# Kernel optimization log

Measured on AMD Instinct MI355X. Metric: run time of the kernel, lower is better.

## Reference

```python
import jax, jax.numpy as jnp
import numpy as np

H = 128; B = 128; NA = 32; N = B * NA; NH = 4; DH = H // NH; F = 2 * H + 3


def _ln(x, g, b, eps=1e-5):
    m = x.mean(-1, keepdims=True)
    v = ((x - m) ** 2).mean(-1, keepdims=True)
    return (x - m) / jnp.sqrt(v + eps) * g + b


def _silu(x):
    return x * jax.nn.sigmoid(x)


def setup_inputs() -> dict:
    key = jax.random.key(0)
    ks = jax.random.split(key, 16)
    def rn(i, shape, s=0.05):
        return jax.random.normal(ks[i], shape, jnp.float32) * s
    return dict(
        num_atoms=jnp.full((B,), NA, dtype=jnp.int32),
        elems=jax.random.randint(ks[0], (N,), 0, 119),
        cell=jnp.tile(10.0 * jnp.eye(3, dtype=jnp.float32), (B, 1)),  # [3B,3]
        coord=jax.random.uniform(ks[1], (N, 3), jnp.float32, 1.0, 9.0),
        emb=rn(2, (119, H), 1.0),
        ln_in_g=jnp.ones((H,), jnp.float32), ln_in_b=jnp.zeros((H,), jnp.float32),
        attn_in_w=rn(3, (H, 3 * H)), attn_in_b=jnp.zeros((3 * H,), jnp.float32),
        attn_out_w=rn(4, (H, H)), attn_out_b=jnp.zeros((H,), jnp.float32),
        ce_w1=rn(5, (3, H)), ce_b1=jnp.zeros((H,), jnp.float32),
        ce_w2=rn(6, (H, H)), ce_b2=jnp.zeros((H,), jnp.float32),
        ln_feat_g=jnp.ones((F,), jnp.float32), ln_feat_b=jnp.zeros((F,), jnp.float32),
        op_w1=rn(7, (F, H)), op_b1=jnp.zeros((H,), jnp.float32),
        op_ln1_g=jnp.ones((H,), jnp.float32), op_ln1_b=jnp.zeros((H,), jnp.float32),
        res_w1=rn(8, (H, H)), res_b1=jnp.zeros((H,), jnp.float32),
        res_ln_g=jnp.ones((H,), jnp.float32), res_ln_b=jnp.zeros((H,), jnp.float32),
        res_w2=rn(9, (H, H)), res_b2=jnp.zeros((H,), jnp.float32),
        op_ln2_g=jnp.ones((H,), jnp.float32), op_ln2_b=jnp.zeros((H,), jnp.float32),
        op_w3=rn(10, (H, 3)), op_b3=jnp.zeros((3,), jnp.float32),
    )


def reference(num_atoms, elems, cell, coord, emb, ln_in_g, ln_in_b,
              attn_in_w, attn_in_b, attn_out_w, attn_out_b,
              ce_w1, ce_b1, ce_w2, ce_b2, ln_feat_g, ln_feat_b,
              op_w1, op_b1, op_ln1_g, op_ln1_b,
              res_w1, res_b1, res_ln_g, res_ln_b, res_w2, res_b2,
              op_ln2_g, op_ln2_b, op_w3, op_b3):
    n = coord.shape[0]
    # atom embedding + input LayerNorm
    x = _ln(emb[elems], ln_in_g, ln_in_b)
    # unbatched multihead self-attention over all atoms (seq_len = n)
    qkv = x @ attn_in_w + attn_in_b
    q, k, v = jnp.split(qkv, 3, axis=-1)
    q = q.reshape(n, NH, DH); k = k.reshape(n, NH, DH); v = v.reshape(n, NH, DH)
    a = jax.nn.softmax(jnp.einsum('qhd,khd->hqk', q, k) / np.float32(np.sqrt(DH)), axis=-1)
    x = jnp.einsum('hqk,khd->qhd', a, v).reshape(n, H) @ attn_out_w + attn_out_b
    # cell encoder on [3B,3] rows
    cf = _silu(cell @ ce_w1 + ce_b1) @ ce_w2 + ce_b2
    bidx = jnp.repeat(jnp.arange(num_atoms.shape[0]), num_atoms, total_repeat_length=n)
    # torch: cf.repeat(B,1)[batch_idx] == cf[batch_idx] since batch_idx < B
    comb = _ln(jnp.concatenate([x, cf[bidx], coord], axis=-1), ln_feat_g, ln_feat_b)
    # offset predictor
    h = _silu(_ln(comb @ op_w1 + op_b1, op_ln1_g, op_ln1_b))
    h = h + (_silu(_ln(h @ res_w1 + res_b1, res_ln_g, res_ln_b)) @ res_w2 + res_b2)
    h = _ln(h, op_ln2_g, op_ln2_b)
    offset = jnp.tanh(h @ op_w3 + op_b3) * 0.01
    perturbed = coord + offset
    # per-molecule clamp: segment gather of per-cell-row min/max replaces the python loop
    c3 = cell.reshape(-1, 3, 3)           # [B,3,3]
    cmin = c3.min(axis=2) + 1e-6          # [B,3]
    cmax = c3.max(axis=2) - 1e-6          # [B,3]
    return jnp.clip(perturbed, cmin[bidx], cmax[bidx])
```

## Files before the change

kernel.cpp:

```cpp
#include <hip/hip_runtime.h>
#include <hip/hip_bf16.h>
#include <math.h>
#include <stdint.h>

#define NATOMS 4096
#define HD     128
#define NHEAD  4
#define DHEAD  32
#define FDIM   259
#define BATCH  128
#define H3X    384
#define SPLIT  4

typedef __attribute__((ext_vector_type(8))) short short8;
typedef __attribute__((ext_vector_type(4))) float float4v;
typedef __attribute__((ext_vector_type(16))) float f32x16;

__device__ __forceinline__ ushort f2bf(float f) {
    uint32_t u = __float_as_uint(f);
    return (ushort)((u + 0x7fffu + ((u >> 16) & 1u)) >> 16);
}
__device__ __forceinline__ float b2f(ushort u) {
    return __uint_as_float(((uint32_t)u) << 16);
}
__device__ __forceinline__ f32x16 z16() {
    f32x16 v;
#pragma unroll
    for (int i = 0; i < 16; i++) v[i] = 0.f;
    return v;
}

__device__ __forceinline__ float blk_sum_128(float v, float* scratch) {
#pragma unroll
    for (int o = 32; o; o >>= 1) v += __shfl_down(v, o);
    int lane = threadIdx.x & 63, w = threadIdx.x >> 6;
    if (lane == 0) scratch[w] = v;
    __syncthreads();
    float r = scratch[0] + scratch[1];
    __syncthreads();
    return r;
}

#define NB_EMB 1024
#define NB_PACK 528
#define NB_CELL 128
__global__ __launch_bounds__(256) void k_setup(
        const int* __restrict__ num_atoms, const float* __restrict__ cell,
        const int* __restrict__ elems, const float* __restrict__ emb,
        const float* __restrict__ ln_in_g, const float* __restrict__ ln_in_b,
        const float* __restrict__ qkvw, const float* __restrict__ aow,
        const float* __restrict__ op1w, const float* __restrict__ r1w,
        const float* __restrict__ r2w,
        const float* __restrict__ ce_w1, const float* __restrict__ ce_b1,
        const float* __restrict__ ce_w2, const float* __restrict__ ce_b2,
        int* __restrict__ bidx, float* __restrict__ cmin, float* __restrict__ cmax,
        ushort* __restrict__ Xb, ushort* __restrict__ Wqkv, ushort* __restrict__ Wao,
        ushort* __restrict__ Wop1, ushort* __restrict__ Wr1, ushort* __restrict__ Wr2,
        float* __restrict__ CF) {
    __shared__ float hs[HD];
    __shared__ int start[BATCH + 1];
    const int t = threadIdx.x, w = t >> 6, lane = t & 63;
    if (blockIdx.x < NB_EMB) {
        int row = blockIdx.x * 4 + w;
        int e = elems[row];
        float v0 = emb[e * HD + lane], v1 = emb[e * HD + 64 + lane];
        float s = v0 + v1, ss = v0 * v0 + v1 * v1;
#pragma unroll
        for (int m = 1; m < 64; m <<= 1) { s += __shfl_xor(s, m); ss += __shfl_xor(ss, m); }
        float mean = s * (1.f / HD);
        float var = ss * (1.f / HD) - mean * mean;
        float inv = rsqrtf(var + 1e-5f);
        Xb[row * HD + lane] = f2bf((v0 - mean) * inv * ln_in_g[lane] + ln_in_b[lane]);
        Xb[row * HD + 64 + lane] = f2bf((v1 - mean) * inv * ln_in_g[64 + lane] + ln_in_b[64 + lane]);
    } else if (blockIdx.x < NB_EMB + NB_PACK) {
        int idx = (blockIdx.x - NB_EMB) * 256 + t;
        if (idx < 49152) {
            int n = idx >> 7, k = idx & 127;
            Wqkv[idx] = f2bf(qkvw[k * H3X + n]);
        } else if (idx < 65536) {
            int j = idx - 49152; int n = j >> 7, k = j & 127;
            Wao[j] = f2bf(aow[k * HD + n]);
        } else if (idx < 102400) {
            int j = idx - 65536; int n = j / 288, k = j - n * 288;
            Wop1[j] = (k < FDIM) ? f2bf(op1w[k * HD + n]) : (ushort)0;
        } else if (idx < 118784) {
            int j = idx - 102400; int n = j >> 7, k = j & 127;
            Wr1[j] = f2bf(r1w[k * HD + n]);
        } else if (idx < 135168) {
            int j = idx - 118784; int n = j >> 7, k = j & 127;
            Wr2[j] = f2bf(r2w[k * HD + n]);
        }
    } else if (blockIdx.x < NB_EMB + NB_PACK + NB_CELL) {
        int r = blockIdx.x - (NB_EMB + NB_PACK);
        if (t < 128) {
            float c0 = cell[r * 3 + 0], c1 = cell[r * 3 + 1], c2 = cell[r * 3 + 2];
            float h = c0 * ce_w1[t] + c1 * ce_w1[HD + t] + c2 * ce_w1[2 * HD + t] + ce_b1[t];
            h = h / (1.f + __expf(-h));
            hs[t] = h;
        }
        __syncthreads();
        if (t < 128) {
            float acc = ce_b2[t];
#pragma unroll 8
            for (int k = 0; k < HD; k++) acc += hs[k] * ce_w2[k * HD + t];
            CF[r * HD + t] = acc;
        }
    } else {
        if (t == 0) {
            int pos = 0;
            for (int b = 0; b < BATCH; b++) { start[b] = pos; pos += num_atoms[b]; }
            start[BATCH] = pos;
        }
        __syncthreads();
        if (t < 128) {
            int s = min(start[t], NATOMS), e = min(start[t + 1], NATOMS);
            for (int j = s; j < e; j++) bidx[j] = t;
            if (t == 0) {
                int total = min(start[BATCH], NATOMS);
                for (int j = total; j < NATOMS; j++) bidx[j] = BATCH - 1;
            }
        }
        for (int rr = t; rr < BATCH * 3; rr += 256) {
            float a0 = cell[rr * 3 + 0], a1 = cell[rr * 3 + 1], a2 = cell[rr * 3 + 2];
            cmin[rr] = fminf(a0, fminf(a1, a2)) + 1e-6f;
            cmax[rr] = fmaxf(a0, fmaxf(a1, a2)) - 1e-6f;
        }
    }
}

__global__ __launch_bounds__(256) void k_qkv(const ushort* __restrict__ A,
                                             const ushort* __restrict__ Wt,
                                             const float* __restrict__ bias,
                                             ushort* __restrict__ Qb, ushort* __restrict__ Kb,
                                             ushort* __restrict__ VTb) {
    __shared__ alignas(16) ushort vt_tmp[4][128][16];
    const int t = threadIdx.x, w = t >> 6, lane = t & 63, quad = lane >> 4, lq = lane & 15;
    const int rowbase = blockIdx.x * 64 + w * 16;
    float4v acc[24];
#pragma unroll
    for (int i = 0; i < 24; i++) acc[i] = (float4v){0.f, 0.f, 0.f, 0.f};
#pragma unroll
    for (int kt = 0; kt < 4; kt++) {
        short8 af = *(const short8*)(A + (rowbase + lq) * HD + kt * 32 + quad * 8);
#pragma unroll
        for (int nt = 0; nt < 24; nt++) {
            short8 wf = *(const short8*)(Wt + (lq + 16 * nt) * HD + kt * 32 + quad * 8);
            acc[nt] = __builtin_amdgcn_mfma_f32_16x16x32_bf16(af, wf, acc[nt], 0, 0, 0);
        }
    }
#pragma unroll
    for (int nt = 0; nt < 24; nt++) {
        int col = lq + 16 * nt;
        float bb = bias[col];
#pragma unroll
        for (int r = 0; r < 4; r++) {
            float c = acc[nt][r] + bb;
            int row = rowbase + quad * 4 + r;
            if (nt < 8) {
                Qb[(((col >> 5) * NATOMS) + row) * 32 + (col & 31)] = f2bf(c * 0.25503487f);
            } else if (nt < 16) {
                int cc = col - 128;
                Kb[(((cc >> 5) * NATOMS) + row) * 32 + (cc & 31)] = f2bf(c);
            } else {
                int cc = col - 256;
                vt_tmp[w][cc][quad * 4 + r] = f2bf(c);
            }
        }
    }
#pragma unroll
    for (int pass = 0; pass < 2; pass++) {
        int cc = lane + 64 * pass;
        int hh = cc >> 5, d = cc & 31;
        uint4 a0 = *(const uint4*)&vt_tmp[w][cc][0];
        uint4 a1 = *(const uint4*)&vt_tmp[w][cc][8];
        ushort* dst = VTb + (size_t)(hh * 32 + d) * NATOMS + rowbase;
        *(uint4*)(dst) = a0;
        *(uint4*)(dst + 8) = a1;
    }
}

__global__ __launch_bounds__(256) void k_attn(const ushort* __restrict__ Qb,
                                              const ushort* __restrict__ Kb,
                                              const ushort* __restrict__ VTb,
                                              ushort* __restrict__ Opart,
                                              float* __restrict__ lpart) {
    __shared__ alignas(16) ushort P_s[4][32 * 72];
    __shared__ alignas(16) float OL[2][32 * 36];
    __shared__ float LL[2][32];
    const int t = threadIdx.x, w = t >> 6, lane = t & 63;
    const int l31 = lane & 31, hi = lane >> 5;
    const int qt = w & 1, kh2 = w >> 1;
    const int h = blockIdx.y, sp = blockIdx.z;
    const int q0 = blockIdx.x * 64;
    const int qrow = q0 + qt * 32 + l31;

    short8 qf0 = *(const short8*)(Qb + (size_t)(h * NATOMS + qrow) * 32 + hi * 8);
    short8 qf1 = *(const short8*)(Qb + (size_t)(h * NATOMS + qrow) * 32 + 16 + hi * 8);
    f32x16 O = z16();
    float lp = 0.f;
    ushort* Pw = &P_s[w][0];
    const int kstart = sp * (NATOMS / SPLIT) + kh2 * 64;

    for (int ck = 0; ck < (NATOMS / SPLIT) / 128; ck++) {
        int kb = kstart + ck * 128;
#pragma unroll
        for (int kt = 0; kt < 2; kt++) {
            int kk = kb + kt * 32;
            const ushort* kp = Kb + (size_t)(h * NATOMS + kk + l31) * 32 + hi * 8;
            short8 kf0 = *(const short8*)(kp);
            short8 kf1 = *(const short8*)(kp + 16);
            f32x16 S = z16();
            S = __builtin_amdgcn_mfma_f32_32x32x16_bf16(kf0, qf0, S, 0, 0, 0);
            S = __builtin_amdgcn_mfma_f32_32x32x16_bf16(kf1, qf1, S, 0, 0, 0);
#pragma unroll
            for (int c = 0; c < 4; c++) {
                float p0 = exp2f(S[4 * c + 0]);
                float p1 = exp2f(S[4 * c + 1]);
                float p2 = exp2f(S[4 * c + 2]);
                float p3 = exp2f(S[4 * c + 3]);
                lp += (p0 + p1) + (p2 + p3);
                uint2 u;
                u.x = (uint32_t)f2bf(p0) | ((uint32_t)f2bf(p1) << 16);
                u.y = (uint32_t)f2bf(p2) | ((uint32_t)f2bf(p3) << 16);
                *(uint2*)(&Pw[l31 * 72 + kt * 32 + c * 8 + hi * 4]) = u;
            }
#pragma unroll
            for (int wd = 0; wd < 2; wd++) {
                int koff = kt * 32 + wd * 16;
                short8 vf = *(const short8*)(VTb + (size_t)(h * 32 + l31) * NATOMS + kb + koff + hi * 8);
                short8 pf = *(const short8*)(&Pw[l31 * 72 + koff + hi * 8]);
                O = __builtin_amdgcn_mfma_f32_32x32x16_bf16(vf, pf, O, 0, 0, 0);
            }
        }
    }
    lp += __shfl_xor(lp, 32);
    if (kh2 == 0) {
#pragma unroll
        for (int c = 0; c < 4; c++) {
            float4 f = {O[4 * c + 0], O[4 * c + 1], O[4 * c + 2], O[4 * c + 3]};
            *(float4*)(&OL[qt][l31 * 36 + c * 8 + hi * 4]) = f;
        }
        if (hi == 0) LL[qt][l31] = lp;
    }
    __syncthreads();
    if (kh2 == 1) {
        lp += LL[qt][l31];
#pragma unroll
        for (int c = 0; c < 4; c++) {
            float4 f = *(const float4*)(&OL[qt][l31 * 36 + c * 8 + hi * 4]);
            float o0 = O[4 * c + 0] + f.x, o1 = O[4 * c + 1] + f.y;
            float o2 = O[4 * c + 2] + f.z, o3 = O[4 * c + 3] + f.w;
            uint2 u;
            u.x = (uint32_t)f2bf(o0) | ((uint32_t)f2bf(o1) << 16);
            u.y = (uint32_t)f2bf(o2) | ((uint32_t)f2bf(o3) << 16);
            *(uint2*)(Opart + (size_t)(sp * NATOMS + qrow) * HD + h * 32 + c * 8 + hi * 4) = u;
        }
        if (hi == 0) lpart[sp * (NHEAD * NATOMS) + h * NATOMS + qrow] = lp;
    }
}

__global__ __launch_bounds__(256) void k_ao(const ushort* __restrict__ Opart,
                                            const float* __restrict__ lpart,
                                            const ushort* __restrict__ Wt,
                                            const float* __restrict__ bias,
                                            ushort* __restrict__ X1b) {
    const int t = threadIdx.x, w = t >> 6, lane = t & 63, quad = lane >> 4, lq = lane & 15;
    const int rowbase = blockIdx.x * 64 + w * 16;
    const int arow = rowbase + lq;
    float4v acc[8];
#pragma unroll
    for (int i = 0; i < 8; i++) acc[i] = (float4v){0.f, 0.f, 0.f, 0.f};
#pragma unroll
    for (int kt = 0; kt < 4; kt++) {
        float l = 0.f;
#pragma unroll
        for (int s = 0; s < SPLIT; s++) l += lpart[s * (NHEAD * NATOMS) + kt * NATOMS + arow];
        float inv = 1.f / l;
        float pv[8];
#pragma unroll
        for (int j = 0; j < 8; j++) pv[j] = 0.f;
#pragma unroll
        for (int s = 0; s < SPLIT; s++) {
            short8 ov = *(const short8*)(Opart + (size_t)(s * NATOMS + arow) * HD + kt * 32 + quad * 8);
#pragma unroll
            for (int j = 0; j < 8; j++) pv[j] += b2f((ushort)ov[j]);
        }
        short8 af;
#pragma unroll
        for (int j = 0; j < 8; j++) af[j] = (short)f2bf(pv[j] * inv);
#pragma unroll
        for (int nt = 0; nt < 8; nt++) {
            short8 wf = *(const short8*)(Wt + (lq + 16 * nt) * HD + kt * 32 + quad * 8);
            acc[nt] = __builtin_amdgcn_mfma_f32_16x16x32_bf16(af, wf, acc[nt], 0, 0, 0);
        }
    }
#pragma unroll
    for (int r = 0; r < 4; r++) {
        int row = rowbase + quad * 4 + r;
#pragma unroll
        for (int nt = 0; nt < 8; nt++)
            X1b[(size_t)row * HD + lq + 16 * nt] = f2bf(acc[nt][r] + bias[lq + 16 * nt]);
    }
}

__global__ void k_comb(const ushort* __restrict__ X1b, const float* __restrict__ CF,
                       const float* __restrict__ coord, const int* __restrict__ bidx,
                       const float* __restrict__ g, const float* __restrict__ b,
                       ushort* __restrict__ COMBb) {
    __shared__ float sc[2];
    int row = blockIdx.x, t = threadIdx.x;
    int bi = bidx[row];
    float v0 = b2f(X1b[row * HD + t]);
    float v1 = CF[bi * HD + t];
    float v2 = (t < 3) ? coord[row * 3 + t] : 0.f;
    float tot = blk_sum_128(v0 + v1 + v2, sc);
    float mean = tot * (1.f / FDIM);
    float d0 = v0 - mean, d1 = v1 - mean, d2 = (t < 3) ? (v2 - mean) : 0.f;
    float var = blk_sum_128(d0 * d0 + d1 * d1 + d2 * d2, sc) * (1.f / FDIM);
    float inv = rsqrtf(var + 1e-5f);
    COMBb[row * 288 + t] = f2bf(d0 * inv * g[t] + b[t]);
    COMBb[row * 288 + 128 + t] = f2bf(d1 * inv * g[128 + t] + b[128 + t]);
    if (t < 3) COMBb[row * 288 + 256 + t] = f2bf(d2 * inv * g[256 + t] + b[256 + t]);
    if (t >= 3 && t < 32) COMBb[row * 288 + 256 + t] = 0;
}

__global__ __launch_bounds__(256) void k_op1(const ushort* __restrict__ A,
                                             const ushort* __restrict__ Wt,
                                             const float* __restrict__ bias,
                                             const float* __restrict__ lg,
                                             const float* __restrict__ lb,
                                             ushort* __restrict__ out) {
    const int t = threadIdx.x, w = t >> 6, lane = t & 63, quad = lane >> 4, lq = lane & 15;
    const int rowbase = blockIdx.x * 64 + w * 16;
    float4v acc[8];
#pragma unroll
    for (int i = 0; i < 8; i++) acc[i] = (float4v){0.f, 0.f, 0.f, 0.f};
#pragma unroll
    for (int kt = 0; kt < 9; kt++) {
        short8 af = *(const short8*)(A + (size_t)(rowbase + lq) * 288 + kt * 32 + quad * 8);
#pragma unroll
        for (int nt = 0; nt < 8; nt++) {
            short8 wf = *(const short8*)(Wt + (size_t)(lq + 16 * nt) * 288 + kt * 32 + quad * 8);
            acc[nt] = __builtin_amdgcn_mfma_f32_16x16x32_bf16(af, wf, acc[nt], 0, 0, 0);
        }
    }
#pragma unroll
    for (int r = 0; r < 4; r++) {
        float c[8], s1 = 0.f, s2 = 0.f;
#pragma unroll
        for (int nt = 0; nt < 8; nt++) {
            c[nt] = acc[nt][r] + bias[lq + 16 * nt];
            s1 += c[nt]; s2 += c[nt] * c[nt];
        }
#pragma unroll
        for (int m = 1; m < 16; m <<= 1) { s1 += __shfl_xor(s1, m); s2 += __shfl_xor(s2, m); }
        float mean = s1 * (1.f / HD);
        float var = s2 * (1.f / HD) - mean * mean;
        float inv = rsqrtf(var + 1e-5f);
        int row = rowbase + quad * 4 + r;
#pragma unroll
        for (int nt = 0; nt < 8; nt++) {
            float o = (c[nt] - mean) * inv * lg[lq + 16 * nt] + lb[lq + 16 * nt];
            o = o / (1.f + __expf(-o));
            out[(size_t)row * HD + lq + 16 * nt] = f2bf(o);
        }
    }
}

__global__ __launch_bounds__(256) void k_tail(const ushort* __restrict__ Hb,
        const ushort* __restrict__ Wr1, const ushort* __restrict__ Wr2,
        const float* __restrict__ r1b, const float* __restrict__ rlg, const float* __restrict__ rlb,
        const float* __restrict__ r2b, const float* __restrict__ l2g, const float* __restrict__ l2b,
        const float* __restrict__ w3, const float* __restrict__ b3,
        const float* __restrict__ coord, const int* __restrict__ bidx,
        const float* __restrict__ cmin, const float* __restrict__ cmax,
        float* __restrict__ out) {
    __shared__ alignas(16) ushort P_s[4][16 * 136];
    const int t = threadIdx.x, w = t >> 6, lane = t & 63, quad = lane >> 4, lq = lane & 15;
    const int rowbase = blockIdx.x * 64 + w * 16;
    ushort* Pw = &P_s[w][0];
    float4v acc[8];
#pragma unroll
    for (int i = 0; i < 8; i++) acc[i] = (float4v){0.f, 0.f, 0.f, 0.f};
#pragma unroll
    for (int kt = 0; kt < 4; kt++) {
        short8 af = *(const short8*)(Hb + (size_t)(rowbase + lq) * HD + kt * 32 + quad * 8);
#pragma unroll
        for (int nt = 0; nt < 8; nt++) {
            short8 wf = *(const short8*)(Wr1 + (size_t)(lq + 16 * nt) * HD + kt * 32 + quad * 8);
            acc[nt] = __builtin_amdgcn_mfma_f32_16x16x32_bf16(af, wf, acc[nt], 0, 0, 0);
        }
    }
#pragma unroll
    for (int r = 0; r < 4; r++) {
        float c[8], s1 = 0.f, s2 = 0.f;
#pragma unroll
        for (int nt = 0; nt < 8; nt++) {
            c[nt] = acc[nt][r] + r1b[lq + 16 * nt];
            s1 += c[nt]; s2 += c[nt] * c[nt];
        }
#pragma unroll
        for (int m = 1; m < 16; m <<= 1) { s1 += __shfl_xor(s1, m); s2 += __shfl_xor(s2, m); }
        float mean = s1 * (1.f / HD);
        float inv = rsqrtf(s2 * (1.f / HD) - mean * mean + 1e-5f);
#pragma unroll
        for (int nt = 0; nt < 8; nt++) {
            float o = (c[nt] - mean) * inv * rlg[lq + 16 * nt] + rlb[lq + 16 * nt];
            o = o / (1.f + __expf(-o));
            Pw[(quad * 4 + r) * 136 + lq + 16 * nt] = f2bf(o);
        }
    }
    float4v acc2[8];
#pragma unroll
    for (int i = 0; i < 8; i++) acc2[i] = (float4v){0.f, 0.f, 0.f, 0.f};
#pragma unroll
    for (int kt = 0; kt < 4; kt++) {
        short8 af = *(const short8*)(&Pw[lq * 136 + kt * 32 + quad * 8]);
#pragma unroll
        for (int nt = 0; nt < 8; nt++) {
            short8 wf = *(const short8*)(Wr2 + (size_t)(lq + 16 * nt) * HD + kt * 32 + quad * 8);
            acc2[nt] = __builtin_amdgcn_mfma_f32_16x16x32_bf16(af, wf, acc2[nt], 0, 0, 0);
        }
    }
#pragma unroll
    for (int r = 0; r < 4; r++) {
        int row = rowbase + quad * 4 + r;
        float c[8], s1 = 0.f, s2 = 0.f;
#pragma unroll
        for (int nt = 0; nt < 8; nt++) {
            c[nt] = acc2[nt][r] + r2b[lq + 16 * nt] + b2f(Hb[(size_t)row * HD + lq + 16 * nt]);
            s1 += c[nt]; s2 += c[nt] * c[nt];
        }
#pragma unroll
        for (int m = 1; m < 16; m <<= 1) { s1 += __shfl_xor(s1, m); s2 += __shfl_xor(s2, m); }
        float mean = s1 * (1.f / HD);
        float inv = rsqrtf(s2 * (1.f / HD) - mean * mean + 1e-5f);
        float t0 = 0.f, t1 = 0.f, t2 = 0.f;
#pragma unroll
        for (int nt = 0; nt < 8; nt++) {
            int col = lq + 16 * nt;
            float h2 = (c[nt] - mean) * inv * l2g[col] + l2b[col];
            t0 += h2 * w3[col * 3 + 0];
            t1 += h2 * w3[col * 3 + 1];
            t2 += h2 * w3[col * 3 + 2];
        }
#pragma unroll
        for (int m = 1; m < 16; m <<= 1) {
            t0 += __shfl_xor(t0, m); t1 += __shfl_xor(t1, m); t2 += __shfl_xor(t2, m);
        }
        if (lq < 3) {
            float sv = (lq == 0) ? t0 : ((lq == 1) ? t1 : t2);
            float off = tanhf(sv + b3[lq]) * 0.01f;
            int bi = bidx[row];
            float pert = coord[row * 3 + lq] + off;
            pert = fminf(fmaxf(pert, cmin[bi * 3 + lq]), cmax[bi * 3 + lq]);
            out[row * 3 + lq] = pert;
        }
    }
}

extern "C" void kernel_launch(void* const* d_in, const int* in_sizes, int n_in,
                              void* d_out, int out_size, void* d_ws, size_t ws_size,
                              hipStream_t stream) {
    const int* num_atoms = (const int*)d_in[0];
    const int* elems = (const int*)d_in[1];
    const float* cell = (const float*)d_in[2];
    const float* coord = (const float*)d_in[3];
    const float* emb = (const float*)d_in[4];
    const float* ln_in_g = (const float*)d_in[5];
    const float* ln_in_b = (const float*)d_in[6];
    const float* attn_in_w = (const float*)d_in[7];
    const float* attn_in_b = (const float*)d_in[8];
    const float* attn_out_w = (const float*)d_in[9];
    const float* attn_out_b = (const float*)d_in[10];
    const float* ce_w1 = (const float*)d_in[11];
    const float* ce_b1 = (const float*)d_in[12];
    const float* ce_w2 = (const float*)d_in[13];
    const float* ce_b2 = (const float*)d_in[14];
    const float* ln_feat_g = (const float*)d_in[15];
    const float* ln_feat_b = (const float*)d_in[16];
    const float* op_w1 = (const float*)d_in[17];
    const float* op_b1 = (const float*)d_in[18];
    const float* op_ln1_g = (const float*)d_in[19];
    const float* op_ln1_b = (const float*)d_in[20];
    const float* res_w1 = (const float*)d_in[21];
    const float* res_b1 = (const float*)d_in[22];
    const float* res_ln_g = (const float*)d_in[23];
    const float* res_ln_b = (const float*)d_in[24];
    const float* res_w2 = (const float*)d_in[25];
    const float* res_b2 = (const float*)d_in[26];
    const float* op_ln2_g = (const float*)d_in[27];
    const float* op_ln2_b = (const float*)d_in[28];
    const float* op_w3 = (const float*)d_in[29];
    const float* op_b3 = (const float*)d_in[30];

    char* ws = (char*)d_ws;
    const size_t MB = 1u << 20;
    ushort* Xb = (ushort*)(ws);
    ushort* X1b = (ushort*)(ws);
    ushort* Qb = (ushort*)(ws + 1 * MB);
    ushort* Kb = (ushort*)(ws + 2 * MB);
    ushort* VTb = (ushort*)(ws + 3 * MB);
    ushort* Opart = (ushort*)(ws + 4 * MB);
    ushort* COMBb = (ushort*)(ws + 4 * MB);
    ushort* Hb = (ushort*)(ws + 6 * MB + (512u << 10));
    float* lpart = (float*)(ws + 8 * MB);
    int* bidx = (int*)(ws + 8 * MB + (256u << 10));
    float* cmin = (float*)(ws + 8 * MB + (272u << 10));
    float* cmax = (float*)(ws + 8 * MB + (274u << 10));
    float* CF = (float*)(ws + 8 * MB + (276u << 10));
    ushort* Wqkv = (ushort*)(ws + 8 * MB + (340u << 10));
    ushort* Wao = (ushort*)(ws + 8 * MB + (436u << 10));
    ushort* Wop1 = (ushort*)(ws + 8 * MB + (468u << 10));
    ushort* Wr1 = (ushort*)(ws + 8 * MB + (540u << 10));
    ushort* Wr2 = (ushort*)(ws + 8 * MB + (572u << 10));

    k_setup<<<NB_EMB + NB_PACK + NB_CELL + 1, 256, 0, stream>>>(
        num_atoms, cell, elems, emb, ln_in_g, ln_in_b,
        attn_in_w, attn_out_w, op_w1, res_w1, res_w2,
        ce_w1, ce_b1, ce_w2, ce_b2,
        bidx, cmin, cmax, Xb, Wqkv, Wao, Wop1, Wr1, Wr2, CF);
    k_qkv<<<64, 256, 0, stream>>>(Xb, Wqkv, attn_in_b, Qb, Kb, VTb);
    k_attn<<<dim3(NATOMS / 64, NHEAD, SPLIT), 256, 0, stream>>>(Qb, Kb, VTb, Opart, lpart);
    k_ao<<<64, 256, 0, stream>>>(Opart, lpart, Wao, attn_out_b, X1b);
    k_comb<<<NATOMS, 128, 0, stream>>>(X1b, CF, coord, bidx, ln_feat_g, ln_feat_b, COMBb);
    k_op1<<<64, 256, 0, stream>>>(COMBb, Wop1, op_b1, op_ln1_g, op_ln1_b, Hb);
    k_tail<<<64, 256, 0, stream>>>(Hb, Wr1, Wr2, res_b1, res_ln_g, res_ln_b,
                                   res_b2, op_ln2_g, op_ln2_b, op_w3, op_b3,
                                   coord, bidx, cmin, cmax, (float*)d_out);
}
```

Before: 214.9 us.

## Fuse embedding LN into QKV and merge post-attention stages into one kernel

Moves the embedding gather and input LayerNorm into the QKV GEMM kernel, which now runs 256 blocks of 16 rows instead of 64 blocks. The attention-output projection, feature concat LayerNorm, op1 layer and residual tail are merged into a single k_back kernel that keeps intermediates in LDS. V is stored in a blocked layout so attention reads contiguous 64-key tiles, and the bf16 packing of P uses byte-permute instructions. This removes several launches and global round-trips at the cost of more LDS syncs per block and smaller per-block tiles.

```diff
diff --git a/kernel.cpp b/kernel.cpp
--- a/kernel.cpp
+++ b/kernel.cpp
@@ -30,50 +30,24 @@
     return v;
 }
 
-__device__ __forceinline__ float blk_sum_128(float v, float* scratch) {
-#pragma unroll
-    for (int o = 32; o; o >>= 1) v += __shfl_down(v, o);
-    int lane = threadIdx.x & 63, w = threadIdx.x >> 6;
-    if (lane == 0) scratch[w] = v;
-    __syncthreads();
-    float r = scratch[0] + scratch[1];
-    __syncthreads();
-    return r;
-}
-
-#define NB_EMB 1024
 #define NB_PACK 528
 #define NB_CELL 128
 __global__ __launch_bounds__(256) void k_setup(
         const int* __restrict__ num_atoms, const float* __restrict__ cell,
-        const int* __restrict__ elems, const float* __restrict__ emb,
-        const float* __restrict__ ln_in_g, const float* __restrict__ ln_in_b,
         const float* __restrict__ qkvw, const float* __restrict__ aow,
         const float* __restrict__ op1w, const float* __restrict__ r1w,
         const float* __restrict__ r2w,
         const float* __restrict__ ce_w1, const float* __restrict__ ce_b1,
         const float* __restrict__ ce_w2, const float* __restrict__ ce_b2,
         int* __restrict__ bidx, float* __restrict__ cmin, float* __restrict__ cmax,
-        ushort* __restrict__ Xb, ushort* __restrict__ Wqkv, ushort* __restrict__ Wao,
+        ushort* __restrict__ Wqkv, ushort* __restrict__ Wao,
         ushort* __restrict__ Wop1, ushort* __restrict__ Wr1, ushort* __restrict__ Wr2,
         float* __restrict__ CF) {
     __shared__ float hs[HD];
     __shared__ int start[BATCH + 1];
-    const int t = threadIdx.x, w = t >> 6, lane = t & 63;
-    if (blockIdx.x < NB_EMB) {
-        int row = blockIdx.x * 4 + w;
-        int e = elems[row];
-        float v0 = emb[e * HD + lane], v1 = emb[e * HD + 64 + lane];
-        float s = v0 + v1, ss = v0 * v0 + v1 * v1;
-#pragma unroll
-        for (int m = 1; m < 64; m <<= 1) { s += __shfl_xor(s, m); ss += __shfl_xor(ss, m); }
-        float mean = s * (1.f / HD);
-        float var = ss * (1.f / HD) - mean * mean;
-        float inv = rsqrtf(var + 1e-5f);
-        Xb[row * HD + lane] = f2bf((v0 - mean) * inv * ln_in_g[lane] + ln_in_b[lane]);
-        Xb[row * HD + 64 + lane] = f2bf((v1 - mean) * inv * ln_in_g[64 + lane] + ln_in_b[64 + lane]);
-    } else if (blockIdx.x < NB_EMB + NB_PACK) {
-        int idx = (blockIdx.x - NB_EMB) * 256 + t;
+    const int t = threadIdx.x;
+    if (blockIdx.x < NB_PACK) {
+        int idx = blockIdx.x * 256 + t;
         if (idx < 49152) {
             int n = idx >> 7, k = idx & 127;
             Wqkv[idx] = f2bf(qkvw[k * H3X + n]);
@@ -90,8 +64,8 @@
             int j = idx - 118784; int n = j >> 7, k = j & 127;
             Wr2[j] = f2bf(r2w[k * HD + n]);
         }
-    } else if (blockIdx.x < NB_EMB + NB_PACK + NB_CELL) {
-        int r = blockIdx.x - (NB_EMB + NB_PACK);
+    } else if (blockIdx.x < NB_PACK + NB_CELL) {
+        int r = blockIdx.x - NB_PACK;
         if (t < 128) {
             float c0 = cell[r * 3 + 0], c1 = cell[r * 3 + 1], c2 = cell[r * 3 + 2];
             float h = c0 * ce_w1[t] + c1 * ce_w1[HD + t] + c2 * ce_w1[2 * HD + t] + ce_b1[t];
@@ -128,52 +102,74 @@
     }
 }
 
-__global__ __launch_bounds__(256) void k_qkv(const ushort* __restrict__ A,
+__global__ __launch_bounds__(256) void k_qkv(const int* __restrict__ elems,
+                                             const float* __restrict__ emb,
+                                             const float* __restrict__ lg,
+                                             const float* __restrict__ lb,
                                              const ushort* __restrict__ Wt,
                                              const float* __restrict__ bias,
                                              ushort* __restrict__ Qb, ushort* __restrict__ Kb,
-                                             ushort* __restrict__ VTb) {
-    __shared__ alignas(16) ushort vt_tmp[4][128][16];
+                                             ushort* __restrict__ VTb2) {
+    __shared__ alignas(16) ushort Af[4][64][8];
+    __shared__ alignas(16) ushort vt[128][16];
     const int t = threadIdx.x, w = t >> 6, lane = t & 63, quad = lane >> 4, lq = lane & 15;
-    const int rowbase = blockIdx.x * 64 + w * 16;
-    float4v acc[24];
-#pragma unroll
-    for (int i = 0; i < 24; i++) acc[i] = (float4v){0.f, 0.f, 0.f, 0.f};
+    const int rb = blockIdx.x * 16;
+    {
+        int row = t >> 4, seg = t & 15;
+        int e = elems[rb + row];
+        const float* ep = emb + (size_t)e * HD + seg * 8;
+        float v[8]; float s = 0.f, ss = 0.f;
+#pragma unroll
+        for (int j = 0; j < 8; j++) { v[j] = ep[j]; s += v[j]; ss += v[j] * v[j]; }
+#pragma unroll
+        for (int m = 1; m < 16; m <<= 1) { s += __shfl_xor(s, m); ss += __shfl_xor(ss, m); }
+        float mean = s * (1.f / HD);
+        float inv = rsqrtf(ss * (1.f / HD) - mean * mean + 1e-5f);
+        ushort o[8];
+#pragma unroll
+        for (int j = 0; j < 8; j++)
+            o[j] = f2bf((v[j] - mean) * inv * lg[seg * 8 + j] + lb[seg * 8 + j]);
+        *(uint4*)&Af[seg >> 2][(seg & 3) * 16 + row][0] = *(uint4*)o;
+    }
+    __syncthreads();
+    float4v acc[6];
+#pragma unroll
+    for (int i = 0; i < 6; i++) acc[i] = (float4v){0.f, 0.f, 0.f, 0.f};
 #pragma unroll
     for (int kt = 0; kt < 4; kt++) {
-        short8 af = *(const short8*)(A + (rowbase + lq) * HD + kt * 32 + quad * 8);
-#pragma unroll
-        for (int nt = 0; nt < 24; nt++) {
-            short8 wf = *(const short8*)(Wt + (lq + 16 * nt) * HD + kt * 32 + quad * 8);
-            acc[nt] = __builtin_amdgcn_mfma_f32_16x16x32_bf16(af, wf, acc[nt], 0, 0, 0);
-        }
-    }
-#pragma unroll
-    for (int nt = 0; nt < 24; nt++) {
-        int col = lq + 16 * nt;
+        short8 af = *(const short8*)&Af[kt][lane][0];
+#pragma unroll
+        for (int i = 0; i < 6; i++) {
+            int nt = w * 6 + i;
+            short8 wf = *(const short8*)(Wt + (size_t)(lq + 16 * nt) * HD + kt * 32 + quad * 8);
+            acc[i] = __builtin_amdgcn_mfma_f32_16x16x32_bf16(af, wf, acc[i], 0, 0, 0);
+        }
+    }
+#pragma unroll
+    for (int i = 0; i < 6; i++) {
+        int col = lq + 16 * (w * 6 + i);
         float bb = bias[col];
 #pragma unroll
         for (int r = 0; r < 4; r++) {
-            float c = acc[nt][r] + bb;
-            int row = rowbase + quad * 4 + r;
-            if (nt < 8) {
-                Qb[(((col >> 5) * NATOMS) + row) * 32 + (col & 31)] = f2bf(c * 0.25503487f);
-            } else if (nt < 16) {
+            float c = acc[i][r] + bb;
+            int rowin = quad * 4 + r;
+            int row = rb + rowin;
+            if (col < 128) {
+                Qb[(size_t)(((col >> 5) * NATOMS) + row) * 32 + (col & 31)] = f2bf(c * 0.25503483f);
+            } else if (col < 256) {
                 int cc = col - 128;
-                Kb[(((cc >> 5) * NATOMS) + row) * 32 + (cc & 31)] = f2bf(c);
+                Kb[(size_t)(((cc >> 5) * NATOMS) + row) * 32 + (cc & 31)] = f2bf(c);
             } else {
-                int cc = col - 256;
-                vt_tmp[w][cc][quad * 4 + r] = f2bf(c);
+                vt[col - 256][rowin] = f2bf(c);
             }
         }
     }
-#pragma unroll
-    for (int pass = 0; pass < 2; pass++) {
-        int cc = lane + 64 * pass;
-        int hh = cc >> 5, d = cc & 31;
-        uint4 a0 = *(const uint4*)&vt_tmp[w][cc][0];
-        uint4 a1 = *(const uint4*)&vt_tmp[w][cc][8];
-        ushort* dst = VTb + (size_t)(hh * 32 + d) * NATOMS + rowbase;
+    __syncthreads();
+    if (t < 128) {
+        int hh = t >> 5, d = t & 31;
+        uint4 a0 = *(const uint4*)&vt[t][0];
+        uint4 a1 = *(const uint4*)&vt[t][8];
+        ushort* dst = VTb2 + ((size_t)(hh * 64 + (rb >> 6)) * 32 + d) * 64 + (rb & 63);
         *(uint4*)(dst) = a0;
         *(uint4*)(dst + 8) = a1;
     }
@@ -181,7 +177,7 @@
 
 __global__ __launch_bounds__(256) void k_attn(const ushort* __restrict__ Qb,
                                               const ushort* __restrict__ Kb,
-                                              const ushort* __restrict__ VTb,
+                                              const ushort* __restrict__ VTb2,
                                               ushort* __restrict__ Opart,
                                               float* __restrict__ lpart) {
     __shared__ alignas(16) ushort P_s[4][32 * 72];
@@ -203,6 +199,7 @@
 
     for (int ck = 0; ck < (NATOMS / SPLIT) / 128; ck++) {
         int kb = kstart + ck * 128;
+        const ushort* vbase = VTb2 + ((size_t)(h * 64 + (kb >> 6)) * 32 + l31) * 64;
 #pragma unroll
         for (int kt = 0; kt < 2; kt++) {
             int kk = kb + kt * 32;
@@ -219,15 +216,19 @@
                 float p2 = exp2f(S[4 * c + 2]);
                 float p3 = exp2f(S[4 * c + 3]);
                 lp += (p0 + p1) + (p2 + p3);
+                uint32_t u0 = __float_as_uint(p0) + 0x8000u;
+                uint32_t u1 = __float_as_uint(p1) + 0x8000u;
+                uint32_t u2 = __float_as_uint(p2) + 0x8000u;
+                uint32_t u3 = __float_as_uint(p3) + 0x8000u;
                 uint2 u;
-                u.x = (uint32_t)f2bf(p0) | ((uint32_t)f2bf(p1) << 16);
-                u.y = (uint32_t)f2bf(p2) | ((uint32_t)f2bf(p3) << 16);
+                u.x = __builtin_amdgcn_perm(u1, u0, 0x07060302u);
+                u.y = __builtin_amdgcn_perm(u3, u2, 0x07060302u);
                 *(uint2*)(&Pw[l31 * 72 + kt * 32 + c * 8 + hi * 4]) = u;
             }
 #pragma unroll
             for (int wd = 0; wd < 2; wd++) {
                 int koff = kt * 32 + wd * 16;
-                short8 vf = *(const short8*)(VTb + (size_t)(h * 32 + l31) * NATOMS + kb + koff + hi * 8);
+                short8 vf = *(const short8*)(vbase + koff + hi * 8);
                 short8 pf = *(const short8*)(&Pw[l31 * 72 + koff + hi * 8]);
                 O = __builtin_amdgcn_mfma_f32_32x32x16_bf16(vf, pf, O, 0, 0, 0);
             }
@@ -259,202 +260,244 @@
     }
 }
 
-__global__ __launch_bounds__(256) void k_ao(const ushort* __restrict__ Opart,
-                                            const float* __restrict__ lpart,
-                                            const ushort* __restrict__ Wt,
-                                            const float* __restrict__ bias,
-                                            ushort* __restrict__ X1b) {
+__global__ __launch_bounds__(256) void k_back(
+        const ushort* __restrict__ Opart, const float* __restrict__ lpart,
+        const ushort* __restrict__ Wao, const float* __restrict__ aob,
+        const float* __restrict__ CF, const float* __restrict__ coord,
+        const int* __restrict__ bidx,
+        const float* __restrict__ fg, const float* __restrict__ fb,
+        const ushort* __restrict__ Wop1, const float* __restrict__ op1b,
+        const float* __restrict__ l1g, const float* __restrict__ l1b,
+        const ushort* __restrict__ Wr1, const float* __restrict__ r1b,
+        const float* __restrict__ rlg, const float* __restrict__ rlb,
+        const ushort* __restrict__ Wr2, const float* __restrict__ r2b,
+        const float* __restrict__ l2g, const float* __restrict__ l2b,
+        const float* __restrict__ w3, const float* __restrict__ b3,
+        const float* __restrict__ cmin, const float* __restrict__ cmax,
+        float* __restrict__ out) {
+    __shared__ alignas(16) ushort AF1[9][64][8];
+    __shared__ alignas(16) ushort AF2[4][64][8];
+    __shared__ alignas(16) ushort AF3[4][64][8];
+    __shared__ float RED[4][16][4];
+    __shared__ float REDC[16][2];
+    __shared__ float COORDS[16][3];
     const int t = threadIdx.x, w = t >> 6, lane = t & 63, quad = lane >> 4, lq = lane & 15;
-    const int rowbase = blockIdx.x * 64 + w * 16;
-    const int arow = rowbase + lq;
-    float4v acc[8];
-#pragma unroll
-    for (int i = 0; i < 8; i++) acc[i] = (float4v){0.f, 0.f, 0.f, 0.f};
-#pragma unroll
-    for (int kt = 0; kt < 4; kt++) {
+    const int rb = blockIdx.x * 16;
+    const int col0 = lq + 32 * w, col1 = col0 + 16;
+
+    const int arow = rb + lq;
+    float4v a0 = {0.f,0.f,0.f,0.f}, a1 = {0.f,0.f,0.f,0.f};
+#pragma unroll
+    for (int h = 0; h < 4; h++) {
         float l = 0.f;
 #pragma unroll
-        for (int s = 0; s < SPLIT; s++) l += lpart[s * (NHEAD * NATOMS) + kt * NATOMS + arow];
+        for (int s = 0; s < SPLIT; s++) l += lpart[s * (NHEAD * NATOMS) + h * NATOMS + arow];
         float inv = 1.f / l;
         float pv[8];
 #pragma unroll
         for (int j = 0; j < 8; j++) pv[j] = 0.f;
 #pragma unroll
         for (int s = 0; s < SPLIT; s++) {
-            short8 ov = *(const short8*)(Opart + (size_t)(s * NATOMS + arow) * HD + kt * 32 + quad * 8);
+            short8 ov = *(const short8*)(Opart + (size_t)(s * NATOMS + arow) * HD + h * 32 + quad * 8);
 #pragma unroll
             for (int j = 0; j < 8; j++) pv[j] += b2f((ushort)ov[j]);
         }
         short8 af;
 #pragma unroll
         for (int j = 0; j < 8; j++) af[j] = (short)f2bf(pv[j] * inv);
-#pragma unroll
-        for (int nt = 0; nt < 8; nt++) {
-            short8 wf = *(const short8*)(Wt + (lq + 16 * nt) * HD + kt * 32 + quad * 8);
-            acc[nt] = __builtin_amdgcn_mfma_f32_16x16x32_bf16(af, wf, acc[nt], 0, 0, 0);
-        }
-    }
-#pragma unroll
-    for (int r = 0; r < 4; r++) {
-        int row = rowbase + quad * 4 + r;
-#pragma unroll
-        for (int nt = 0; nt < 8; nt++)
-            X1b[(size_t)row * HD + lq + 16 * nt] = f2bf(acc[nt][r] + bias[lq + 16 * nt]);
-    }
-}
-
-__global__ void k_comb(const ushort* __restrict__ X1b, const float* __restrict__ CF,
-                       const float* __restrict__ coord, const int* __restrict__ bidx,
-                       const float* __restrict__ g, const float* __restrict__ b,
-                       ushort* __restrict__ COMBb) {
-    __shared__ float sc[2];
-    int row = blockIdx.x, t = threadIdx.x;
-    int bi = bidx[row];
-    float v0 = b2f(X1b[row * HD + t]);
-    float v1 = CF[bi * HD + t];
-    float v2 = (t < 3) ? coord[row * 3 + t] : 0.f;
-    float tot = blk_sum_128(v0 + v1 + v2, sc);
-    float mean = tot * (1.f / FDIM);
-    float d0 = v0 - mean, d1 = v1 - mean, d2 = (t < 3) ? (v2 - mean) : 0.f;
-    float var = blk_sum_128(d0 * d0 + d1 * d1 + d2 * d2, sc) * (1.f / FDIM);
-    float inv = rsqrtf(var + 1e-5f);
-    COMBb[row * 288 + t] = f2bf(d0 * inv * g[t] + b[t]);
-    COMBb[row * 288 + 128 + t] = f2bf(d1 * inv * g[128 + t] + b[128 + t]);
-    if (t < 3) COMBb[row * 288 + 256 + t] = f2bf(d2 * inv * g[256 + t] + b[256 + t]);
-    if (t >= 3 && t < 32) COMBb[row * 288 + 256 + t] = 0;
-}
-
-__global__ __launch_bounds__(256) void k_op1(const ushort* __restrict__ A,
-                                             const ushort* __restrict__ Wt,
-                                             const float* __restrict__ bias,
-                                             const float* __restrict__ lg,
-                                             const float* __restrict__ lb,
-                                             ushort* __restrict__ out) {
-    const int t = threadIdx.x, w = t >> 6, lane = t & 63, quad = lane >> 4, lq = lane & 15;
-    const int rowbase = blockIdx.x * 64 + w * 16;
-    float4v acc[8];
-#pragma unroll
-    for (int i = 0; i < 8; i++) acc[i] = (float4v){0.f, 0.f, 0.f, 0.f};
+        short8 w0 = *(const short8*)(Wao + (size_t)col0 * HD + h * 32 + quad * 8);
+        short8 w1 = *(const short8*)(Wao + (size_t)col1 * HD + h * 32 + quad * 8);
+        a0 = __builtin_amdgcn_mfma_f32_16x16x32_bf16(af, w0, a0, 0, 0, 0);
+        a1 = __builtin_amdgcn_mfma_f32_16x16x32_bf16(af, w1, a1, 0, 0, 0);
+    }
+    float x1[2][4];
+#pragma unroll
+    for (int r = 0; r < 4; r++) { x1[0][r] = a0[r] + aob[col0]; x1[1][r] = a1[r] + aob[col1]; }
+
+    float cfv[2][4];
+#pragma unroll
+    for (int r = 0; r < 4; r++) {
+        int bi = bidx[rb + quad * 4 + r];
+        cfv[0][r] = CF[bi * HD + col0];
+        cfv[1][r] = CF[bi * HD + col1];
+    }
+#pragma unroll
+    for (int r = 0; r < 4; r++) {
+        float s1 = x1[0][r] + x1[1][r] + cfv[0][r] + cfv[1][r];
+        float s2 = x1[0][r]*x1[0][r] + x1[1][r]*x1[1][r] + cfv[0][r]*cfv[0][r] + cfv[1][r]*cfv[1][r];
+#pragma unroll
+        for (int m = 1; m < 16; m <<= 1) { s1 += __shfl_xor(s1, m); s2 += __shfl_xor(s2, m); }
+        if (lq == 0) { RED[w][quad * 4 + r][0] = s1; RED[w][quad * 4 + r][1] = s2; }
+    }
+    if (t < 16) {
+        float c0 = coord[(rb + t) * 3 + 0], c1 = coord[(rb + t) * 3 + 1], c2 = coord[(rb + t) * 3 + 2];
+        COORDS[t][0] = c0; COORDS[t][1] = c1; COORDS[t][2] = c2;
+        REDC[t][0] = c0 + c1 + c2; REDC[t][1] = c0*c0 + c1*c1 + c2*c2;
+    }
+    if (t < 64) { uint4 z = {0,0,0,0}; *(uint4*)&AF1[8][t][0] = z; }
+    __syncthreads();
+    {
+#pragma unroll
+        for (int r = 0; r < 4; r++) {
+            int ri = quad * 4 + r;
+            float s1 = RED[0][ri][0] + RED[1][ri][0] + RED[2][ri][0] + RED[3][ri][0] + REDC[ri][0];
+            float s2 = RED[0][ri][1] + RED[1][ri][1] + RED[2][ri][1] + RED[3][ri][1] + REDC[ri][1];
+            float mn = s1 * (1.f / FDIM);
+            float iv = rsqrtf(s2 * (1.f / FDIM) - mn * mn + 1e-5f);
+#pragma unroll
+            for (int i = 0; i < 2; i++) {
+                int c = i ? col1 : col0;
+                float vx = ((i ? x1[1][r] : x1[0][r]) - mn) * iv * fg[c] + fb[c];
+                float vc = ((i ? cfv[1][r] : cfv[0][r]) - mn) * iv * fg[c + 128] + fb[c + 128];
+                AF1[c >> 5][((c >> 3) & 3) * 16 + ri][c & 7] = f2bf(vx);
+                int c2 = c + 128;
+                AF1[c2 >> 5][((c2 >> 3) & 3) * 16 + ri][c2 & 7] = f2bf(vc);
+            }
+        }
+        if (t < 16) {
+            float s1 = RED[0][t][0] + RED[1][t][0] + RED[2][t][0] + RED[3][t][0] + REDC[t][0];
+            float s2 = RED[0][t][1] + RED[1][t][1] + RED[2][t][1] + RED[3][t][1] + REDC[t][1];
+            float mn = s1 * (1.f / FDIM);
+            float iv = rsqrtf(s2 * (1.f / FDIM) - mn * mn + 1e-5f);
+#pragma unroll
+            for (int c = 0; c < 3; c++)
+                AF1[8][t][c] = f2bf((COORDS[t][c] - mn) * iv * fg[256 + c] + fb[256 + c]);
+        }
+    }
+    __syncthreads();
+
+    float4v c0v = {0.f,0.f,0.f,0.f}, c1v = {0.f,0.f,0.f,0.f};
 #pragma unroll
     for (int kt = 0; kt < 9; kt++) {
-        short8 af = *(const short8*)(A + (size_t)(rowbase + lq) * 288 + kt * 32 + quad * 8);
-#pragma unroll
-        for (int nt = 0; nt < 8; nt++) {
-            short8 wf = *(const short8*)(Wt + (size_t)(lq + 16 * nt) * 288 + kt * 32 + quad * 8);
-            acc[nt] = __builtin_amdgcn_mfma_f32_16x16x32_bf16(af, wf, acc[nt], 0, 0, 0);
-        }
-    }
-#pragma unroll
-    for (int r = 0; r < 4; r++) {
-        float c[8], s1 = 0.f, s2 = 0.f;
-#pragma unroll
-        for (int nt = 0; nt < 8; nt++) {
-            c[nt] = acc[nt][r] + bias[lq + 16 * nt];
-            s1 += c[nt]; s2 += c[nt] * c[nt];
-        }
+        short8 af = *(const short8*)&AF1[kt][lane][0];
+        short8 w0 = *(const short8*)(Wop1 + (size_t)col0 * 288 + kt * 32 + quad * 8);
+        short8 w1 = *(const short8*)(Wop1 + (size_t)col1 * 288 + kt * 32 + quad * 8);
+        c0v = __builtin_amdgcn_mfma_f32_16x16x32_bf16(af, w0, c0v, 0, 0, 0);
+        c1v = __builtin_amdgcn_mfma_f32_16x16x32_bf16(af, w1, c1v, 0, 0, 0);
+    }
+    float h0[4], h1[4];
+#pragma unroll
+    for (int r = 0; r < 4; r++) {
+        h0[r] = c0v[r] + op1b[col0]; h1[r] = c1v[r] + op1b[col1];
+        float s1 = h0[r] + h1[r], s2 = h0[r]*h0[r] + h1[r]*h1[r];
 #pragma unroll
         for (int m = 1; m < 16; m <<= 1) { s1 += __shfl_xor(s1, m); s2 += __shfl_xor(s2, m); }
-        float mean = s1 * (1.f / HD);
-        float var = s2 * (1.f / HD) - mean * mean;
-        float inv = rsqrtf(var + 1e-5f);
-        int row = rowbase + quad * 4 + r;
-#pragma unroll
-        for (int nt = 0; nt < 8; nt++) {
-            float o = (c[nt] - mean) * inv * lg[lq + 16 * nt] + lb[lq + 16 * nt];
+        if (lq == 0) { RED[w][quad * 4 + r][0] = s1; RED[w][quad * 4 + r][1] = s2; }
+    }
+    __syncthreads();
+#pragma unroll
+    for (int r = 0; r < 4; r++) {
+        int ri = quad * 4 + r;
+        float s1 = RED[0][ri][0] + RED[1][ri][0] + RED[2][ri][0] + RED[3][ri][0];
+        float s2 = RED[0][ri][1] + RED[1][ri][1] + RED[2][ri][1] + RED[3][ri][1];
+        float mn = s1 * (1.f / HD);
+        float iv = rsqrtf(s2 * (1.f / HD) - mn * mn + 1e-5f);
+#pragma unroll
+        for (int i = 0; i < 2; i++) {
+            int c = i ? col1 : col0;
+            float o = ((i ? h1[r] : h0[r]) - mn) * iv * l1g[c] + l1b[c];
             o = o / (1.f + __expf(-o));
-            out[(size_t)row * HD + lq + 16 * nt] = f2bf(o);
-        }
-    }
-}
-
-__global__ __launch_bounds__(256) void k_tail(const ushort* __restrict__ Hb,
-        const ushort* __restrict__ Wr1, const ushort* __restrict__ Wr2,
-        const float* __restrict__ r1b, const float* __restrict__ rlg, const float* __restrict__ rlb,
-        const float* __restrict__ r2b, const float* __restrict__ l2g, const float* __restrict__ l2b,
-        const float* __restrict__ w3, const float* __restrict__ b3,
-        const float* __restrict__ coord, const int* __restrict__ bidx,
-        const float* __restrict__ cmin, const float* __restrict__ cmax,
-        float* __restrict__ out) {
-    __shared__ alignas(16) ushort P_s[4][16 * 136];
-    const int t = threadIdx.x, w = t >> 6, lane = t & 63, quad = lane >> 4, lq = lane & 15;
-    const int rowbase = blockIdx.x * 64 + w * 16;
-    ushort* Pw = &P_s[w][0];
-    float4v acc[8];
-#pragma unroll
-    for (int i = 0; i < 8; i++) acc[i] = (float4v){0.f, 0.f, 0.f, 0.f};
+            AF2[c >> 5][((c >> 3) & 3) * 16 + ri][c & 7] = f2bf(o);
+        }
+    }
+    __syncthreads();
+
+    float4v d0v = {0.f,0.f,0.f,0.f}, d1v = {0.f,0.f,0.f,0.f};
 #pragma unroll
     for (int kt = 0; kt < 4; kt++) {
-        short8 af = *(const short8*)(Hb + (size_t)(rowbase + lq) * HD + kt * 32 + quad * 8);
-#pragma unroll
-        for (int nt = 0; nt < 8; nt++) {
-            short8 wf = *(const short8*)(Wr1 + (size_t)(lq + 16 * nt) * HD + kt * 32 + quad * 8);
-            acc[nt] = __builtin_amdgcn_mfma_f32_16x16x32_bf16(af, wf, acc[nt], 0, 0, 0);
-        }
-    }
-#pragma unroll
-    for (int r = 0; r < 4; r++) {
-        float c[8], s1 = 0.f, s2 = 0.f;
-#pragma unroll
-        for (int nt = 0; nt < 8; nt++) {
-            c[nt] = acc[nt][r] + r1b[lq + 16 * nt];
-            s1 += c[nt]; s2 += c[nt] * c[nt];
-        }
+        short8 af = *(const short8*)&AF2[kt][lane][0];
+        short8 w0 = *(const short8*)(Wr1 + (size_t)col0 * HD + kt * 32 + quad * 8);
+        short8 w1 = *(const short8*)(Wr1 + (size_t)col1 * HD + kt * 32 + quad * 8);
+        d0v = __builtin_amdgcn_mfma_f32_16x16x32_bf16(af, w0, d0v, 0, 0, 0);
+        d1v = __builtin_amdgcn_mfma_f32_16x16x32_bf16(af, w1, d1v, 0, 0, 0);
+    }
+    float e0[4], e1[4];
+#pragma unroll
+    for (int r = 0; r < 4; r++) {
+        e0[r] = d0v[r] + r1b[col0]; e1[r] = d1v[r] + r1b[col1];
+        float s1 = e0[r] + e1[r], s2 = e0[r]*e0[r] + e1[r]*e1[r];
 #pragma unroll
         for (int m = 1; m < 16; m <<= 1) { s1 += __shfl_xor(s1, m); s2 += __shfl_xor(s2, m); }
-        float mean = s1 * (1.f / HD);
-        float inv = rsqrtf(s2 * (1.f / HD) - mean * mean + 1e-5f);
-#pragma unroll
-        for (int nt = 0; nt < 8; nt++) {
-            float o = (c[nt] - mean) * inv * rlg[lq + 16 * nt] + rlb[lq + 16 * nt];
+        if (lq == 0) { RED[w][quad * 4 + r][0] = s1; RED[w][quad * 4 + r][1] = s2; }
+    }
+    __syncthreads();
+#pragma unroll
+    for (int r = 0; r < 4; r++) {
+        int ri = quad * 4 + r;
+        float s1 = RED[0][ri][0] + RED[1][ri][0] + RED[2][ri][0] + RED[3][ri][0];
+        float s2 = RED[0][ri][1] + RED[1][ri][1] + RED[2][ri][1] + RED[3][ri][1];
+        float mn = s1 * (1.f / HD);
+        float iv = rsqrtf(s2 * (1.f / HD) - mn * mn + 1e-5f);
+#pragma unroll
+        for (int i = 0; i < 2; i++) {
+            int c = i ? col1 : col0;
+            float o = ((i ? e1[r] : e0[r]) - mn) * iv * rlg[c] + rlb[c];
             o = o / (1.f + __expf(-o));
-            Pw[(quad * 4 + r) * 136 + lq + 16 * nt] = f2bf(o);
-        }
-    }
-    float4v acc2[8];
-#pragma unroll
-    for (int i = 0; i < 8; i++) acc2[i] = (float4v){0.f, 0.f, 0.f, 0.f};
+            AF3[c >> 5][((c >> 3) & 3) * 16 + ri][c & 7] = f2bf(o);
+        }
+    }
+    __syncthreads();
+
+    float4v f0v = {0.f,0.f,0.f,0.f}, f1v = {0.f,0.f,0.f,0.f};
 #pragma unroll
     for (int kt = 0; kt < 4; kt++) {
-        short8 af = *(const short8*)(&Pw[lq * 136 + kt * 32 + quad * 8]);
-#pragma unroll
-        for (int nt = 0; nt < 8; nt++) {
-            short8 wf = *(const short8*)(Wr2 + (size_t)(lq + 16 * nt) * HD + kt * 32 + quad * 8);
-            acc2[nt] = __builtin_amdgcn_mfma_f32_16x16x32_bf16(af, wf, acc2[nt], 0, 0, 0);
-        }
-    }
-#pragma unroll
-    for (int r = 0; r < 4; r++) {
-        int row = rowbase + quad * 4 + r;
-        float c[8], s1 = 0.f, s2 = 0.f;
-#pragma unroll
-        for (int nt = 0; nt < 8; nt++) {
-            c[nt] = acc2[nt][r] + r2b[lq + 16 * nt] + b2f(Hb[(size_t)row * HD + lq + 16 * nt]);
-            s1 += c[nt]; s2 += c[nt] * c[nt];
-        }
+        short8 af = *(const short8*)&AF3[kt][lane][0];
+        short8 w0 = *(const short8*)(Wr2 + (size_t)col0 * HD + kt * 32 + quad * 8);
+        short8 w1 = *(const short8*)(Wr2 + (size_t)col1 * HD + kt * 32 + quad * 8);
+        f0v = __builtin_amdgcn_mfma_f32_16x16x32_bf16(af, w0, f0v, 0, 0, 0);
+        f1v = __builtin_amdgcn_mfma_f32_16x16x32_bf16(af, w1, f1v, 0, 0, 0);
+    }
+    float g0r[4], g1r[4];
+#pragma unroll
+    for (int r = 0; r < 4; r++) {
+        int ri = quad * 4 + r;
+        float rs0 = b2f(AF2[col0 >> 5][((col0 >> 3) & 3) * 16 + ri][col0 & 7]);
+        float rs1 = b2f(AF2[col1 >> 5][((col1 >> 3) & 3) * 16 + ri][col1 & 7]);
+        g0r[r] = f0v[r] + r2b[col0] + rs0;
+        g1r[r] = f1v[r] + r2b[col1] + rs1;
+        float s1 = g0r[r] + g1r[r], s2 = g0r[r]*g0r[r] + g1r[r]*g1r[r];
 #pragma unroll
         for (int m = 1; m < 16; m <<= 1) { s1 += __shfl_xor(s1, m); s2 += __shfl_xor(s2, m); }
-        float mean = s1 * (1.f / HD);
-        float inv = rsqrtf(s2 * (1.f / HD) - mean * mean + 1e-5f);
-        float t0 = 0.f, t1 = 0.f, t2 = 0.f;
-#pragma unroll
-        for (int nt = 0; nt < 8; nt++) {
-            int col = lq + 16 * nt;
-            float h2 = (c[nt] - mean) * inv * l2g[col] + l2b[col];
-            t0 += h2 * w3[col * 3 + 0];
-            t1 += h2 * w3[col * 3 + 1];
-            t2 += h2 * w3[col * 3 + 2];
-        }
-#pragma unroll
-        for (int m = 1; m < 16; m <<= 1) {
-            t0 += __shfl_xor(t0, m); t1 += __shfl_xor(t1, m); t2 += __shfl_xor(t2, m);
-        }
-        if (lq < 3) {
-            float sv = (lq == 0) ? t0 : ((lq == 1) ? t1 : t2);
-            float off = tanhf(sv + b3[lq]) * 0.01f;
-            int bi = bidx[row];
-            float pert = coord[row * 3 + lq] + off;
-            pert = fminf(fmaxf(pert, cmin[bi * 3 + lq]), cmax[bi * 3 + lq]);
-            out[row * 3 + lq] = pert;
+        if (lq == 0) { RED[w][ri][0] = s1; RED[w][ri][1] = s2; }
+    }
+    __syncthreads();
+    float tp[4][3];
+#pragma unroll
+    for (int r = 0; r < 4; r++) {
+        int ri = quad * 4 + r;
+        float s1 = RED[0][ri][0] + RED[1][ri][0] + RED[2][ri][0] + RED[3][ri][0];
+        float s2 = RED[0][ri][1] + RED[1][ri][1] + RED[2][ri][1] + RED[3][ri][1];
+        float mn = s1 * (1.f / HD);
+        float iv = rsqrtf(s2 * (1.f / HD) - mn * mn + 1e-5f);
+        float h20 = (g0r[r] - mn) * iv * l2g[col0] + l2b[col0];
+        float h21 = (g1r[r] - mn) * iv * l2g[col1] + l2b[col1];
+#pragma unroll
+        for (int c = 0; c < 3; c++) {
+            float v = h20 * w3[col0 * 3 + c] + h21 * w3[col1 * 3 + c];
+#pragma unroll
+            for (int m = 1; m < 16; m <<= 1) v += __shfl_xor(v, m);
+            tp[r][c] = v;
+        }
+    }
+    __syncthreads();
+    if (lq == 0) {
+#pragma unroll
+        for (int r = 0; r < 4; r++) {
+            RED[w][quad * 4 + r][0] = tp[r][0];
+            RED[w][quad * 4 + r][1] = tp[r][1];
+            RED[w][quad * 4 + r][2] = tp[r][2];
+        }
+    }
+    __syncthreads();
+    if (t < 16) {
+        int bi = bidx[rb + t];
+#pragma unroll
+        for (int c = 0; c < 3; c++) {
+            float sv = RED[0][t][c] + RED[1][t][c] + RED[2][t][c] + RED[3][t][c];
+            float off = tanhf(sv + b3[c]) * 0.01f;
+            float pert = COORDS[t][c] + off;
+            pert = fminf(fmaxf(pert, cmin[bi * 3 + c]), cmax[bi * 3 + c]);
+            out[(rb + t) * 3 + c] = pert;
         }
     }
 }
@@ -496,36 +539,31 @@
 
     char* ws = (char*)d_ws;
     const size_t MB = 1u << 20;
-    ushort* Xb = (ushort*)(ws);
-    ushort* X1b = (ushort*)(ws);
-    ushort* Qb = (ushort*)(ws + 1 * MB);
-    ushort* Kb = (ushort*)(ws + 2 * MB);
-    ushort* VTb = (ushort*)(ws + 3 * MB);
-    ushort* Opart = (ushort*)(ws + 4 * MB);
-    ushort* COMBb = (ushort*)(ws + 4 * MB);
-    ushort* Hb = (ushort*)(ws + 6 * MB + (512u << 10));
-    float* lpart = (float*)(ws + 8 * MB);
-    int* bidx = (int*)(ws + 8 * MB + (256u << 10));
-    float* cmin = (float*)(ws + 8 * MB + (272u << 10));
-    float* cmax = (float*)(ws + 8 * MB + (274u << 10));
-    float* CF = (float*)(ws + 8 * MB + (276u << 10));
-    ushort* Wqkv = (ushort*)(ws + 8 * MB + (340u << 10));
-    ushort* Wao = (ushort*)(ws + 8 * MB + (436u << 10));
-    ushort* Wop1 = (ushort*)(ws + 8 * MB + (468u << 10));
-    ushort* Wr1 = (ushort*)(ws + 8 * MB + (540u << 10));
-    ushort* Wr2 = (ushort*)(ws + 8 * MB + (572u << 10));
-
-    k_setup<<<NB_EMB + NB_PACK + NB_CELL + 1, 256, 0, stream>>>(
-        num_atoms, cell, elems, emb, ln_in_g, ln_in_b,
-        attn_in_w, attn_out_w, op_w1, res_w1, res_w2,
+    ushort* Qb = (ushort*)(ws);
+    ushort* Kb = (ushort*)(ws + 1 * MB);
+    ushort* VTb2 = (ushort*)(ws + 2 * MB);
+    ushort* Opart = (ushort*)(ws + 3 * MB);
+    float* lpart = (float*)(ws + 7 * MB);
+    int* bidx = (int*)(ws + 7 * MB + (256u << 10));
+    float* cmin = (float*)(ws + 7 * MB + (272u << 10));
+    float* cmax = (float*)(ws + 7 * MB + (274u << 10));
+    float* CF = (float*)(ws + 7 * MB + (276u << 10));
+    ushort* Wqkv = (ushort*)(ws + 7 * MB + (340u << 10));
+    ushort* Wao = (ushort*)(ws + 7 * MB + (436u << 10));
+    ushort* Wop1 = (ushort*)(ws + 7 * MB + (468u << 10));
+    ushort* Wr1 = (ushort*)(ws + 7 * MB + (540u << 10));
+    ushort* Wr2 = (ushort*)(ws + 7 * MB + (572u << 10));
+
+    k_setup<<<NB_PACK + NB_CELL + 1, 256, 0, stream>>>(
+        num_atoms, cell, attn_in_w, attn_out_w, op_w1, res_w1, res_w2,
         ce_w1, ce_b1, ce_w2, ce_b2,
-        bidx, cmin, cmax, Xb, Wqkv, Wao, Wop1, Wr1, Wr2, CF);
-    k_qkv<<<64, 256, 0, stream>>>(Xb, Wqkv, attn_in_b, Qb, Kb, VTb);
-    k_attn<<<dim3(NATOMS / 64, NHEAD, SPLIT), 256, 0, stream>>>(Qb, Kb, VTb, Opart, lpart);
-    k_ao<<<64, 256, 0, stream>>>(Opart, lpart, Wao, attn_out_b, X1b);
-    k_comb<<<NATOMS, 128, 0, stream>>>(X1b, CF, coord, bidx, ln_feat_g, ln_feat_b, COMBb);
-    k_op1<<<64, 256, 0, stream>>>(COMBb, Wop1, op_b1, op_ln1_g, op_ln1_b, Hb);
-    k_tail<<<64, 256, 0, stream>>>(Hb, Wr1, Wr2, res_b1, res_ln_g, res_ln_b,
-                                   res_b2, op_ln2_g, op_ln2_b, op_w3, op_b3,
-                                   coord, bidx, cmin, cmax, (float*)d_out);
-}
+        bidx, cmin, cmax, Wqkv, Wao, Wop1, Wr1, Wr2, CF);
+    k_qkv<<<256, 256, 0, stream>>>(elems, emb, ln_in_g, ln_in_b, Wqkv, attn_in_b,
+                                   Qb, Kb, VTb2);
+    k_attn<<<dim3(NATOMS / 64, NHEAD, SPLIT), 256, 0, stream>>>(Qb, Kb, VTb2, Opart, lpart);
+    k_back<<<256, 256, 0, stream>>>(Opart, lpart, Wao, attn_out_b, CF, coord, bidx,
+                                    ln_feat_g, ln_feat_b, Wop1, op_b1, op_ln1_g, op_ln1_b,
+                                    Wr1, res_b1, res_ln_g, res_ln_b, Wr2, res_b2,
+                                    op_ln2_g, op_ln2_b, op_w3, op_b3, cmin, cmax,
+                                    (float*)d_out);
+}
```

New measurement: 179.4 us. -16.5%, faster.
